# Performance work log

Measured on AMD Instinct MI355X. Metric: run time of the kernel, lower is better.

Reference implementation:

```python
import jax, jax.numpy as jnp
import numpy as np
from jax import lax

SIGMA = 0.5
SCORE_THRESHOLD = 0.05
N = 4096


def setup_inputs() -> dict:
    key = jax.random.key(0)
    k1, k2, k3 = jax.random.split(key, 3)
    # realistic boxes: top-left corner in [0,1000), width/height in [1,101)
    xy1 = jax.random.uniform(k1, (N, 2), dtype=jnp.float32) * 1000.0
    wh = jax.random.uniform(k2, (N, 2), dtype=jnp.float32) * 100.0 + 1.0
    boxes = jnp.concatenate([xy1, xy1 + wh], axis=1)  # [N,4] x1,y1,x2,y2
    scores = jax.random.uniform(k3, (N,), dtype=jnp.float32)
    return {"boxes": boxes, "scores": scores}


def _soft_nms(boxes, scores, sigma, score_threshold):
    n = boxes.shape[0]
    areas = (boxes[:, 2] - boxes[:, 0]) * (boxes[:, 3] - boxes[:, 1])  # [N]
    idx_range = jnp.arange(n)

    def body(i, state):
        s, processed = state
        # pick highest-score unprocessed box (== swap-to-front in the
        # original sorted formulation)
        masked = jnp.where(processed, -jnp.inf, s)
        j = jnp.argmax(masked)
        b = boxes[j]
        # IoU of selected box vs all boxes (vectorized)
        xx1 = jnp.maximum(b[0], boxes[:, 0])
        yy1 = jnp.maximum(b[1], boxes[:, 1])
        xx2 = jnp.minimum(b[2], boxes[:, 2])
        yy2 = jnp.minimum(b[3], boxes[:, 3])
        w = jnp.maximum(xx2 - xx1, 0.0)
        h = jnp.maximum(yy2 - yy1, 0.0)
        inter = w * h
        iou = inter / (areas[j] + areas - inter)
        # Gaussian decay on remaining (unprocessed) boxes
        weight = jnp.exp(-(iou * iou) / sigma)
        active = (~processed) & (idx_range != j)
        s = jnp.where(active, s * weight, s)
        processed = processed.at[j].set(True)
        return s, processed

    scores_out, _ = lax.fori_loop(
        0, n, body, (scores, jnp.zeros((n,), dtype=bool)))
    keep = scores_out > score_threshold
    return scores_out, keep


def reference(boxes, scores):
    return _soft_nms(boxes, scores, SIGMA, SCORE_THRESHOLD)
```

## Files before the change

kernel.cpp:

```cpp
#include <hip/hip_runtime.h>

#define N_BOX 4096
#define NT    1024
#define KPT   4
#define NW    16
#define KTOP  8
#define MAXC  (NW * KTOP)
#define NEG_INF (-__builtin_huge_valf())

typedef unsigned long long u64;

__device__ __forceinline__ u64 dpp_max_u64(u64 x) {
#define DPP_STEP(CTRL) { \
    int lo_ = __builtin_amdgcn_update_dpp(0, (int)(unsigned)x,         CTRL, 0xF, 0xF, true); \
    int hi_ = __builtin_amdgcn_update_dpp(0, (int)(unsigned)(x >> 32), CTRL, 0xF, 0xF, true); \
    u64 o_ = ((u64)(unsigned)hi_ << 32) | (unsigned)lo_; \
    x = (o_ > x) ? o_ : x; }
    DPP_STEP(0x111)
    DPP_STEP(0x112)
    DPP_STEP(0x114)
    DPP_STEP(0x118)
    DPP_STEP(0x142)
    DPP_STEP(0x143)
#undef DPP_STEP
    const int lo = __builtin_amdgcn_readlane((int)(unsigned)x, 63);
    const int hi = __builtin_amdgcn_readlane((int)(unsigned)(x >> 32), 63);
    return ((u64)(unsigned)hi << 32) | (unsigned)lo;
}

__device__ __forceinline__ float bcast_f32(float v, int ln) {
    return __int_as_float(__builtin_amdgcn_readlane(__float_as_int(v), ln));
}

__global__ __launch_bounds__(NT, 1) void soft_nms_kernel(
    const float* __restrict__ boxes,
    const float* __restrict__ scores,
    float* __restrict__ out)
{
    const int tid  = threadIdx.x;
    const int lane = tid & 63;
    const int wave = tid >> 6;

    __shared__ unsigned s_key[N_BOX];
    __shared__ u64      s_wtop[NW][KTOP + 1];
    __shared__ float    s_wgeom[NW][KTOP][5];
    __shared__ int      s_cmt[MAXC];
    __shared__ int      s_C;

    #pragma unroll
    for (int k = 0; k < KPT; ++k) {
        const int i = tid * KPT + k;
        const float4 b = reinterpret_cast<const float4*>(boxes)[i];
        const float cx = 0.5f * (b.x + b.z);
        const float cy = 0.5f * (b.y + b.w);
        int icx = (int)(cx * 0.016f); icx = icx < 0 ? 0 : (icx > 15 ? 15 : icx);
        int icy = (int)(cy * 0.016f); icy = icy < 0 ? 0 : (icy > 15 ? 15 : icy);
        unsigned m = 0;
        #pragma unroll
        for (int bb = 0; bb < 4; ++bb)
            m |= (((unsigned)(icx >> bb) & 1u) << (2*bb)) |
                 (((unsigned)(icy >> bb) & 1u) << (2*bb + 1));
        s_key[i] = (m << 12) | (unsigned)i;
    }
    __syncthreads();

    for (int kk = 2; kk <= N_BOX; kk <<= 1) {
        for (int j = kk >> 1; j > 0; j >>= 1) {
            #pragma unroll
            for (int t = 0; t < KPT; ++t) {
                const int e = tid + t * NT;
                const int p = e ^ j;
                if (p > e) {
                    const unsigned a = s_key[e], b = s_key[p];
                    const bool up = ((e & kk) == 0);
                    if ((a > b) == up) { s_key[e] = b; s_key[p] = a; }
                }
            }
            __syncthreads();
        }
    }

    float bx1[KPT], by1[KPT], bx2[KPT], by2[KPT], bar[KPT], cur[KPT], fin[KPT];
    unsigned klo[KPT];
    #pragma unroll
    for (int k = 0; k < KPT; ++k) {
        const int spos = tid * KPT + k;
        const int oi = (int)(s_key[spos] & 0xFFFu);
        const float4 b = reinterpret_cast<const float4*>(boxes)[oi];
        bx1[k] = b.x; by1[k] = b.y; bx2[k] = b.z; by2[k] = b.w;
        bar[k] = (b.z - b.x) * (b.w - b.y);
        cur[k] = scores[oi];
        fin[k] = 0.0f;
        klo[k] = ((unsigned)(4095 - oi) << 13) | (unsigned)(spos + 1);
    }

    float tbx1 = bx1[0], tby1 = by1[0], tbx2 = bx2[0], tby2 = by2[0];
    #pragma unroll
    for (int k = 1; k < KPT; ++k) {
        tbx1 = fminf(tbx1, bx1[k]); tby1 = fminf(tby1, by1[k]);
        tbx2 = fmaxf(tbx2, bx2[k]); tby2 = fmaxf(tby2, by2[k]);
    }
    float wbx1 = tbx1, wby1 = tby1, wbx2 = tbx2, wby2 = tby2;
    #pragma unroll
    for (int off = 1; off < 64; off <<= 1) {
        wbx1 = fminf(wbx1, __shfl_xor(wbx1, off));
        wby1 = fminf(wby1, __shfl_xor(wby1, off));
        wbx2 = fmaxf(wbx2, __shfl_xor(wbx2, off));
        wby2 = fmaxf(wby2, __shfl_xor(wby2, off));
    }

    auto rebuild = [&]() {
        u64 lk[KPT];
        #pragma unroll
        for (int k = 0; k < KPT; ++k)
            lk[k] = (cur[k] < 0.0f) ? 0ull
                  : (((u64)__float_as_uint(cur[k]) << 25) | (u64)klo[k]);
        #pragma unroll
        for (int p = 0; p <= KTOP; ++p) {
            u64 m4 = lk[0];
            #pragma unroll
            for (int k = 1; k < KPT; ++k) m4 = lk[k] > m4 ? lk[k] : m4;
            const u64 m = dpp_max_u64(m4);
            if (lane == 0) s_wtop[wave][p] = m;
            if (p < KTOP && m != 0ull) {
                #pragma unroll
                for (int k = 0; k < KPT; ++k) {
                    if (lk[k] == m) {
                        lk[k] = 0ull;
                        s_wgeom[wave][p][0] = bx1[k];
                        s_wgeom[wave][p][1] = by1[k];
                        s_wgeom[wave][p][2] = bx2[k];
                        s_wgeom[wave][p][3] = by2[k];
                        s_wgeom[wave][p][4] = bar[k];
                    }
                }
            }
        }
    };

    rebuild();
    __syncthreads();

    int remaining = N_BOX;
    int guard = 0;
    while (remaining > 0 && ++guard <= N_BOX) {
        if (wave == 0) {
            const int cw = lane >> 2, cr = lane & 3;
            u64 ck0 = s_wtop[cw][cr];
            u64 ck1 = s_wtop[cw][4 + cr];
            const float c0x1 = s_wgeom[cw][cr][0],   c0y1 = s_wgeom[cw][cr][1];
            const float c0x2 = s_wgeom[cw][cr][2],   c0y2 = s_wgeom[cw][cr][3];
            const float c0ar = s_wgeom[cw][cr][4];
            const float c1x1 = s_wgeom[cw][4+cr][0], c1y1 = s_wgeom[cw][4+cr][1];
            const float c1x2 = s_wgeom[cw][4+cr][2], c1y2 = s_wgeom[cw][4+cr][3];
            const float c1ar = s_wgeom[cw][4+cr][4];
            u64 tv = (lane < NW) ? s_wtop[lane][KTOP] : 0ull;
            const u64 T = dpp_max_u64(tv);
            int C = 0;
            while (C < MAXC) {
                u64 m4 = ck0 > ck1 ? ck0 : ck1;
                const u64 m = dpp_max_u64(m4);
                if (m <= T) break;
                const u64 b0 = __ballot(ck0 == m);
                int ln; bool r1;
                if (b0) { ln = (int)__ffsll(b0) - 1; r1 = false; }
                else    { ln = (int)__ffsll(__ballot(ck1 == m)) - 1; r1 = true; }
                const int slot = (ln >> 2) * KTOP + (r1 ? 4 : 0) + (ln & 3);
                if (lane == 0) s_cmt[C] = (slot << 12) | (int)((m & 0x1FFFull) - 1);
                if (ck0 == m) ck0 = 0ull;
                if (ck1 == m) ck1 = 0ull;
                const float jx1 = bcast_f32(r1 ? c1x1 : c0x1, ln);
                const float jy1 = bcast_f32(r1 ? c1y1 : c0y1, ln);
                const float jx2 = bcast_f32(r1 ? c1x2 : c0x2, ln);
                const float jy2 = bcast_f32(r1 ? c1y2 : c0y2, ln);
                const float ja  = bcast_f32(r1 ? c1ar : c0ar, ln);
#define DECAY_CK(CK, CX1, CY1, CX2, CY2, CAR) \
                if (CK != 0ull) { \
                    const float xx1 = fmaxf(jx1, CX1), yy1 = fmaxf(jy1, CY1); \
                    const float xx2 = fminf(jx2, CX2), yy2 = fminf(jy2, CY2); \
                    const float w_ = fmaxf(xx2 - xx1, 0.0f), h_ = fmaxf(yy2 - yy1, 0.0f); \
                    const float inter = w_ * h_; \
                    if (inter > 0.0f) { \
                        const float iou = inter / (ja + CAR - inter); \
                        float s_ = __uint_as_float((unsigned)(CK >> 25)); \
                        s_ *= __expf(iou * iou * -2.0f); \
                        CK = ((u64)__float_as_uint(s_) << 25) | (CK & 0x1FFFFFFull); } }
                DECAY_CK(ck0, c0x1, c0y1, c0x2, c0y2, c0ar)
                DECAY_CK(ck1, c1x1, c1y1, c1x2, c1y2, c1ar)
#undef DECAY_CK
                ++C;
            }
            if (lane == 0) s_C = C;
        }
        __syncthreads();

        const int C = s_C;
        bool wdirty = false;
        for (int t = 0; t < C; ++t) {
            const int rec  = s_cmt[t];
            const int slot = rec >> 12;
            const int sp   = rec & 0xFFF;
            const float jx1 = s_wgeom[slot >> 3][slot & 7][0];
            const float jy1 = s_wgeom[slot >> 3][slot & 7][1];
            const float jx2 = s_wgeom[slot >> 3][slot & 7][2];
            const float jy2 = s_wgeom[slot >> 3][slot & 7][3];
            const float ja  = s_wgeom[slot >> 3][slot & 7][4];
            if (jx1 > wbx2 || jx2 < wbx1 || jy1 > wby2 || jy2 < wby1) continue;
            wdirty = true;
            const bool mine = (sp >> 2) == tid;
            if (!mine && (jx1 > tbx2 || jx2 < tbx1 || jy1 > tby2 || jy2 < tby1))
                continue;
            #pragma unroll
            for (int k = 0; k < KPT; ++k) {
                if (mine && (sp & 3) == k) {
                    fin[k] = cur[k];
                    cur[k] = NEG_INF;
                } else {
                    const float xx1 = fmaxf(jx1, bx1[k]);
                    const float yy1 = fmaxf(jy1, by1[k]);
                    const float xx2 = fminf(jx2, bx2[k]);
                    const float yy2 = fminf(jy2, by2[k]);
                    const float w = fmaxf(xx2 - xx1, 0.0f);
                    const float h = fmaxf(yy2 - yy1, 0.0f);
                    const float inter = w * h;
                    const float iou = inter / (ja + bar[k] - inter);
                    cur[k] *= __expf(iou * iou * -2.0f);
                }
            }
        }
        __syncthreads();
        if (wdirty) rebuild();
        __syncthreads();
        remaining -= C;
    }

    #pragma unroll
    for (int k = 0; k < KPT; ++k) {
        const int oi = 4095 - (int)((klo[k] >> 13) & 0xFFFu);
        out[oi] = fin[k];
        out[N_BOX + oi] = (fin[k] > 0.05f) ? 1.0f : 0.0f;
    }
}

extern "C" void kernel_launch(void* const* d_in, const int* in_sizes, int n_in,
                              void* d_out, int out_size, void* d_ws, size_t ws_size,
                              hipStream_t stream) {
    const float* boxes  = (const float*)d_in[0];
    const float* scores = (const float*)d_in[1];
    float* out = (float*)d_out;
    soft_nms_kernel<<<1, NT, 0, stream>>>(boxes, scores, out);
}
```

Baseline: 3.404 ms.

## Double-buffer per-wave top-K tables and compact committed list per wave

The per-wave top candidate tables become double-buffered, so the rebuild writes the alternate buffer. This lets one of the two __syncthreads per round be dropped. Each wave first filters the committed boxes in parallel with a ballot against its bounding box and builds a compacted list, so the serial decay loop visits only overlapping commits. Waves with no overlapping commits copy their table to the other buffer instead of rebuilding, which adds some LDS use and copy traffic.

Result: faster. 2.878 ms, median of 2 (-15.5%).

```diff
diff --git a/kernel.cpp b/kernel.cpp
--- a/kernel.cpp
+++ b/kernel.cpp
@@ -42,9 +42,10 @@
     const int wave = tid >> 6;
 
     __shared__ unsigned s_key[N_BOX];
-    __shared__ u64      s_wtop[NW][KTOP + 1];
-    __shared__ float    s_wgeom[NW][KTOP][5];
+    __shared__ u64      s_wtop[2][NW][KTOP + 1];
+    __shared__ float    s_wgeom[2][NW][KTOP][5];
     __shared__ int      s_cmt[MAXC];
+    __shared__ int      s_wlist[NW][MAXC];
     __shared__ int      s_C;
 
     #pragma unroll
@@ -109,7 +110,7 @@
         wby2 = fmaxf(wby2, __shfl_xor(wby2, off));
     }
 
-    auto rebuild = [&]() {
+    auto rebuild = [&](int G) {
         u64 lk[KPT];
         #pragma unroll
         for (int k = 0; k < KPT; ++k)
@@ -121,24 +122,25 @@
             #pragma unroll
             for (int k = 1; k < KPT; ++k) m4 = lk[k] > m4 ? lk[k] : m4;
             const u64 m = dpp_max_u64(m4);
-            if (lane == 0) s_wtop[wave][p] = m;
+            if (lane == 0) s_wtop[G][wave][p] = m;
             if (p < KTOP && m != 0ull) {
                 #pragma unroll
                 for (int k = 0; k < KPT; ++k) {
                     if (lk[k] == m) {
                         lk[k] = 0ull;
-                        s_wgeom[wave][p][0] = bx1[k];
-                        s_wgeom[wave][p][1] = by1[k];
-                        s_wgeom[wave][p][2] = bx2[k];
-                        s_wgeom[wave][p][3] = by2[k];
-                        s_wgeom[wave][p][4] = bar[k];
+                        s_wgeom[G][wave][p][0] = bx1[k];
+                        s_wgeom[G][wave][p][1] = by1[k];
+                        s_wgeom[G][wave][p][2] = bx2[k];
+                        s_wgeom[G][wave][p][3] = by2[k];
+                        s_wgeom[G][wave][p][4] = bar[k];
                     }
                 }
             }
         }
     };
 
-    rebuild();
+    rebuild(0);
+    int g = 0;
     __syncthreads();
 
     int remaining = N_BOX;
@@ -146,15 +148,15 @@
     while (remaining > 0 && ++guard <= N_BOX) {
         if (wave == 0) {
             const int cw = lane >> 2, cr = lane & 3;
-            u64 ck0 = s_wtop[cw][cr];
-            u64 ck1 = s_wtop[cw][4 + cr];
-            const float c0x1 = s_wgeom[cw][cr][0],   c0y1 = s_wgeom[cw][cr][1];
-            const float c0x2 = s_wgeom[cw][cr][2],   c0y2 = s_wgeom[cw][cr][3];
-            const float c0ar = s_wgeom[cw][cr][4];
-            const float c1x1 = s_wgeom[cw][4+cr][0], c1y1 = s_wgeom[cw][4+cr][1];
-            const float c1x2 = s_wgeom[cw][4+cr][2], c1y2 = s_wgeom[cw][4+cr][3];
-            const float c1ar = s_wgeom[cw][4+cr][4];
-            u64 tv = (lane < NW) ? s_wtop[lane][KTOP] : 0ull;
+            u64 ck0 = s_wtop[g][cw][cr];
+            u64 ck1 = s_wtop[g][cw][4 + cr];
+            const float c0x1 = s_wgeom[g][cw][cr][0],   c0y1 = s_wgeom[g][cw][cr][1];
+            const float c0x2 = s_wgeom[g][cw][cr][2],   c0y2 = s_wgeom[g][cw][cr][3];
+            const float c0ar = s_wgeom[g][cw][cr][4];
+            const float c1x1 = s_wgeom[g][cw][4+cr][0], c1y1 = s_wgeom[g][cw][4+cr][1];
+            const float c1x2 = s_wgeom[g][cw][4+cr][2], c1y2 = s_wgeom[g][cw][4+cr][3];
+            const float c1ar = s_wgeom[g][cw][4+cr][4];
+            u64 tv = (lane < NW) ? s_wtop[g][lane][KTOP] : 0ull;
             const u64 T = dpp_max_u64(tv);
             int C = 0;
             while (C < MAXC) {
@@ -195,18 +197,36 @@
         __syncthreads();
 
         const int C = s_C;
-        bool wdirty = false;
-        for (int t = 0; t < C; ++t) {
-            const int rec  = s_cmt[t];
+
+        int myn = 0;
+        for (int t0 = 0; t0 < C; t0 += 64) {
+            const int t = t0 + lane;
+            bool pred = false;
+            if (t < C) {
+                const int slot = s_cmt[t] >> 12;
+                const float jx1 = s_wgeom[g][slot >> 3][slot & 7][0];
+                const float jy1 = s_wgeom[g][slot >> 3][slot & 7][1];
+                const float jx2 = s_wgeom[g][slot >> 3][slot & 7][2];
+                const float jy2 = s_wgeom[g][slot >> 3][slot & 7][3];
+                pred = !(jx1 > wbx2 || jx2 < wbx1 || jy1 > wby2 || jy2 < wby1);
+            }
+            const u64 mask = __ballot(pred);
+            if (pred) {
+                const int pos = myn + (int)__popcll(mask & ((1ull << lane) - 1ull));
+                s_wlist[wave][pos] = t;
+            }
+            myn += (int)__popcll(mask);
+        }
+
+        for (int n = 0; n < myn; ++n) {
+            const int rec  = s_cmt[s_wlist[wave][n]];
             const int slot = rec >> 12;
             const int sp   = rec & 0xFFF;
-            const float jx1 = s_wgeom[slot >> 3][slot & 7][0];
-            const float jy1 = s_wgeom[slot >> 3][slot & 7][1];
-            const float jx2 = s_wgeom[slot >> 3][slot & 7][2];
-            const float jy2 = s_wgeom[slot >> 3][slot & 7][3];
-            const float ja  = s_wgeom[slot >> 3][slot & 7][4];
-            if (jx1 > wbx2 || jx2 < wbx1 || jy1 > wby2 || jy2 < wby1) continue;
-            wdirty = true;
+            const float jx1 = s_wgeom[g][slot >> 3][slot & 7][0];
+            const float jy1 = s_wgeom[g][slot >> 3][slot & 7][1];
+            const float jx2 = s_wgeom[g][slot >> 3][slot & 7][2];
+            const float jy2 = s_wgeom[g][slot >> 3][slot & 7][3];
+            const float ja  = s_wgeom[g][slot >> 3][slot & 7][4];
             const bool mine = (sp >> 2) == tid;
             if (!mine && (jx1 > tbx2 || jx2 < tbx1 || jy1 > tby2 || jy2 < tby1))
                 continue;
@@ -228,10 +248,18 @@
                 }
             }
         }
+
+        if (myn > 0) {
+            rebuild(g ^ 1);
+        } else {
+            if (lane <= KTOP) s_wtop[g ^ 1][wave][lane] = s_wtop[g][wave][lane];
+            if (lane < KTOP * 5)
+                ((float*)s_wgeom[g ^ 1][wave])[lane] =
+                    ((const float*)s_wgeom[g][wave])[lane];
+        }
+        g ^= 1;
+        remaining -= C;
         __syncthreads();
-        if (wdirty) rebuild();
-        __syncthreads();
-        remaining -= C;
     }
 
     #pragma unroll
```
